# Optimization experiments

Hardware: AMD Instinct MI355X
Metric: run time of the kernel (lower is better)

The kernel has to match this reference:

```python
import jax, jax.numpy as jnp
import numpy as np

D, N, H, DK, DFF, L = 1024, 2048, 8, 128, 4096, 4
LAM = 1.0 / float(np.sqrt(DK))  # attention scale (layer.lam)


def setup_inputs() -> dict:
    key = jax.random.key(0)
    ks = jax.random.split(key, 6)
    s = 1.0 / float(np.sqrt(D))
    X = jax.random.normal(ks[0], (D, N), jnp.float32)
    Q = jax.random.normal(ks[1], (L, H, DK, D), jnp.float32) * s
    K = jax.random.normal(ks[2], (L, H, DK, D), jnp.float32) * s
    V = jax.random.normal(ks[3], (L, H, D, D), jnp.float32) * s
    W1 = jax.random.normal(ks[4], (L, DFF, D), jnp.float32) * s
    b1 = jnp.zeros((L, DFF, 1), jnp.float32)
    W2 = jax.random.normal(ks[5], (L, D, DFF), jnp.float32) * (1.0 / float(np.sqrt(DFF)))
    b2 = jnp.zeros((L, D, 1), jnp.float32)
    return {"X": X, "Q": Q, "K": K, "V": V, "W1": W1, "b1": b1, "W2": W2, "b2": b2}


def _layer(X, p):
    Q, K, V, W1, b1, W2, b2 = p
    # Batched multi-head attention; original loops heads and sums outputs.
    QX = jnp.einsum('hkd,dn->hkn', Q, X)          # [H, DK, N]
    KX = jnp.einsum('hkd,dn->hkn', K, X)          # [H, DK, N]
    scores = jnp.einsum('hkn,hkm->hnm', QX, KX) * LAM  # [H, N, N]
    A = jax.nn.softmax(scores, axis=1)            # torch softmax(dim=0) over [N, N]
    VX = jnp.einsum('hed,dn->hen', V, X)          # [H, D, N]
    Y = jnp.einsum('hen,hnm->em', VX, A)          # sum over heads -> [D, N]
    X = X + Y
    Hh = jax.nn.relu(W1 @ X + b1)                 # [DFF, N]
    return X + W2 @ Hh + b2


def reference(X, Q, K, V, W1, b1, W2, b2):
    def step(carry, p):
        return _layer(carry, p), None
    Xf, _ = jax.lax.scan(step, X, (Q, K, V, W1, b1, W2, b2))
    return Xf
```

## Files before the change

kernel.cpp:

```cpp
#include <hip/hip_runtime.h>

typedef unsigned short u16;
typedef _Float16 f16;
typedef _Float16 fh8 __attribute__((ext_vector_type(8)));
typedef float f32x4 __attribute__((ext_vector_type(4)));

#define cD   1024
#define cN   2048
#define cH   8
#define cDK  128
#define cDFF 4096
#define cL   4
#define LAM_ 0.08838834764831845f
#define QKSC 64.0f

__device__ __forceinline__ u16 f2h(float f) {
    union { f16 h; u16 u; } x; x.h = (f16)f; return x.u;
}
__device__ __forceinline__ float h2f(u16 u) {
    union { u16 u; f16 h; } x; x.u = u; return (float)x.h;
}
__device__ __forceinline__ void split_fh(float v, u16& h, u16& l) {
    h = f2h(v);
    l = f2h(v - h2f(h));
}

__device__ __forceinline__ void async_cp16(const u16* gsrc, u16* ldst) {
    __builtin_amdgcn_global_load_lds(
        (const __attribute__((address_space(1))) unsigned int*)gsrc,
        (__attribute__((address_space(3))) unsigned int*)(unsigned int)(unsigned long long)ldst,
        16, 0, 0);
}

__global__ void cast_split4(const float* __restrict__ s, u16* __restrict__ h,
                            u16* __restrict__ l, int n4, float sc) {
    int i = blockIdx.x * 256 + threadIdx.x;
    if (i < n4) {
        float4 v = ((const float4*)s)[i];
        v.x *= sc; v.y *= sc; v.z *= sc; v.w *= sc;
        ushort4 hh, ll;
        split_fh(v.x, hh.x, ll.x);
        split_fh(v.y, hh.y, ll.y);
        split_fh(v.z, hh.z, ll.z);
        split_fh(v.w, hh.w, ll.w);
        ((ushort4*)h)[i] = hh;
        if (l) ((ushort4*)l)[i] = ll;
    }
}

__global__ __launch_bounds__(256)
void transpose_f32(const float* __restrict__ in, float* __restrict__ out, int R, int C) {
    __shared__ float t[32][33];
    const int bx = blockIdx.x * 32;
    const int by = blockIdx.y * 32;
    const int tx = threadIdx.x & 31, ty = threadIdx.x >> 5;
#pragma unroll
    for (int yy = 0; yy < 32; yy += 8)
        t[ty + yy][tx] = in[(long)(by + ty + yy) * C + bx + tx];
    __syncthreads();
#pragma unroll
    for (int yy = 0; yy < 32; yy += 8)
        out[(long)(bx + ty + yy) * R + by + tx] = t[tx][ty + yy];
}

__global__ __launch_bounds__(256)
void softmax_rows(const float* __restrict__ S, u16* __restrict__ Ph) {
    const long base = (long)blockIdx.x * cN;
    const float4* s4 = (const float4*)(S + base);
    const int tid = threadIdx.x;
    float4 v0 = s4[tid];
    float4 v1 = s4[tid + 256];
    float mx = fmaxf(fmaxf(fmaxf(v0.x, v0.y), fmaxf(v0.z, v0.w)),
                     fmaxf(fmaxf(v1.x, v1.y), fmaxf(v1.z, v1.w)));
    __shared__ float rm[256], rl[256];
    rm[tid] = mx; __syncthreads();
    for (int w = 128; w > 0; w >>= 1) {
        if (tid < w) rm[tid] = fmaxf(rm[tid], rm[tid + w]);
        __syncthreads();
    }
    mx = rm[0];
    float l = __expf(v0.x - mx) + __expf(v0.y - mx) + __expf(v0.z - mx) + __expf(v0.w - mx)
            + __expf(v1.x - mx) + __expf(v1.y - mx) + __expf(v1.z - mx) + __expf(v1.w - mx);
    rl[tid] = l; __syncthreads();
    for (int w = 128; w > 0; w >>= 1) {
        if (tid < w) rl[tid] += rl[tid + w];
        __syncthreads();
    }
    const float inv = 1.0f / rl[0];
    ushort4 a, b;
    a.x = f2h(__expf(v0.x - mx) * inv);
    a.y = f2h(__expf(v0.y - mx) * inv);
    a.z = f2h(__expf(v0.z - mx) * inv);
    a.w = f2h(__expf(v0.w - mx) * inv);
    b.x = f2h(__expf(v1.x - mx) * inv);
    b.y = f2h(__expf(v1.y - mx) * inv);
    b.z = f2h(__expf(v1.z - mx) * inv);
    b.w = f2h(__expf(v1.w - mx) * inv);
    ((ushort4*)(Ph + base))[tid] = a;
    ((ushort4*)(Ph + base))[tid + 256] = b;
}

template<int ALO, int BLO, int DBUF>
__global__ __launch_bounds__(256)
void gemm_split(const u16* __restrict__ Ah, const u16* __restrict__ Al, int lda, long bsA,
                const u16* __restrict__ Bh, const u16* __restrict__ Bl, int ldb, long bsB,
                float* __restrict__ Cf, u16* __restrict__ Cbh, u16* __restrict__ Cbl,
                int ldc, long bsC,
                int M, int N, int K, int SK,
                float alpha, int mode, int relu, const float* __restrict__ biasN)
{
    const int g = blockIdx.z / SK;
    const int s = blockIdx.z % SK;
    const long za = (long)g * bsA + (long)s * K;
    const long zb = (long)g * bsB + (long)s * K;
    Ah += za; Bh += zb;
    if constexpr (ALO) Al += za;
    if constexpr (BLO) Bl += zb;
    if (s != 0) biasN = nullptr;

    __shared__ __align__(16) u16 Ash[128 * 32];
    __shared__ __align__(16) u16 Bsh[128 * 32];
    __shared__ __align__(16) u16 Asl[ALO ? 128 * 32 : 8];
    __shared__ __align__(16) u16 Bsl[BLO ? 128 * 32 : 8];
    __shared__ __align__(16) u16 Ash1[DBUF ? 128 * 32 : 8];
    __shared__ __align__(16) u16 Bsh1[DBUF ? 128 * 32 : 8];

    const int tid  = threadIdx.x;
    const int lane = tid & 63;
    const int wave = tid >> 6;
    const int wm = (wave >> 1) * 64;
    const int wn = (wave & 1) * 64;

    const int nbx = gridDim.x;
    const int nwg = nbx * (int)gridDim.y;
    int wg = blockIdx.y * nbx + blockIdx.x;
    {
        const int qq = nwg >> 3, rr = nwg & 7;
        const int xcd = wg & 7, lid = wg >> 3;
        wg = (xcd < rr ? xcd * (qq + 1) : rr * (qq + 1) + (xcd - rr) * qq) + lid;
    }
    const int m0 = (wg / nbx) * 128;
    const int n0 = (wg % nbx) * 128;

    const int srow = lane >> 2;
    const int scol = (((lane & 3) ^ (srow & 3)) * 8);
    const int q = lane >> 4;
    const int r = lane & 15;
    const int fcol = ((q ^ (r & 3)) * 8);

    f32x4 acc[4][4];
#pragma unroll
    for (int i = 0; i < 4; ++i)
#pragma unroll
        for (int j = 0; j < 4; ++j)
            acc[i][j] = f32x4{0.f, 0.f, 0.f, 0.f};

    if constexpr (DBUF) {
        auto stage = [&](u16* SA, u16* SB, int k0) {
#pragma unroll
            for (int p = 0; p < 2; ++p) {
                const int c = p * 4 + wave;
                const int grow = c * 16 + srow;
                async_cp16(Ah + (long)(m0 + grow) * lda + k0 + scol, SA + c * 512);
                async_cp16(Bh + (long)(n0 + grow) * ldb + k0 + scol, SB + c * 512);
            }
        };
        auto compute = [&](const u16* SA, const u16* SB) {
            fh8 af[4], bf[4];
#pragma unroll
            for (int i = 0; i < 4; ++i) af[i] = *(const fh8*)(SA + (wm + i * 16 + r) * 32 + fcol);
#pragma unroll
            for (int j = 0; j < 4; ++j) bf[j] = *(const fh8*)(SB + (wn + j * 16 + r) * 32 + fcol);
#pragma unroll
            for (int i = 0; i < 4; ++i)
#pragma unroll
                for (int j = 0; j < 4; ++j)
                    acc[i][j] = __builtin_amdgcn_mfma_f32_16x16x32_f16(af[i], bf[j], acc[i][j], 0, 0, 0);
        };

        stage(Ash, Bsh, 0);
        for (int k0 = 0; k0 < K; k0 += 64) {
            stage(Ash1, Bsh1, k0 + 32);
            asm volatile("s_waitcnt vmcnt(4)" ::: "memory");
            __builtin_amdgcn_s_barrier();
            asm volatile("" ::: "memory");
            compute(Ash, Bsh);
            asm volatile("" ::: "memory");
            __builtin_amdgcn_s_barrier();
            if (k0 + 64 < K) {
                stage(Ash, Bsh, k0 + 64);
                asm volatile("s_waitcnt vmcnt(4)" ::: "memory");
            } else {
                asm volatile("s_waitcnt vmcnt(0)" ::: "memory");
            }
            __builtin_amdgcn_s_barrier();
            asm volatile("" ::: "memory");
            compute(Ash1, Bsh1);
            asm volatile("" ::: "memory");
            __builtin_amdgcn_s_barrier();
        }
    } else {
        for (int k0 = 0; k0 < K; k0 += 32) {
#pragma unroll
            for (int p = 0; p < 2; ++p) {
                const int c = p * 4 + wave;
                const int grow = c * 16 + srow;
                const long aoff = (long)(m0 + grow) * lda + k0 + scol;
                const long boff = (long)(n0 + grow) * ldb + k0 + scol;
                async_cp16(Ah + aoff, Ash + c * 512);
                if constexpr (ALO) async_cp16(Al + aoff, Asl + c * 512);
                async_cp16(Bh + boff, Bsh + c * 512);
                if constexpr (BLO) async_cp16(Bl + boff, Bsl + c * 512);
            }
            __syncthreads();

            fh8 afh[4], afl[4], bfh[4], bfl[4];
#pragma unroll
            for (int i = 0; i < 4; ++i) {
                const int ra = (wm + i * 16 + r) * 32 + fcol;
                afh[i] = *(const fh8*)(Ash + ra);
                if constexpr (ALO) afl[i] = *(const fh8*)(Asl + ra);
            }
#pragma unroll
            for (int j = 0; j < 4; ++j) {
                const int rb = (wn + j * 16 + r) * 32 + fcol;
                bfh[j] = *(const fh8*)(Bsh + rb);
                if constexpr (BLO) bfl[j] = *(const fh8*)(Bsl + rb);
            }
#pragma unroll
            for (int i = 0; i < 4; ++i)
#pragma unroll
                for (int j = 0; j < 4; ++j) {
                    acc[i][j] = __builtin_amdgcn_mfma_f32_16x16x32_f16(afh[i], bfh[j], acc[i][j], 0, 0, 0);
                    if constexpr (BLO)
                        acc[i][j] = __builtin_amdgcn_mfma_f32_16x16x32_f16(afh[i], bfl[j], acc[i][j], 0, 0, 0);
                    if constexpr (ALO)
                        acc[i][j] = __builtin_amdgcn_mfma_f32_16x16x32_f16(afl[i], bfh[j], acc[i][j], 0, 0, 0);
                }
            __syncthreads();
        }
    }

#pragma unroll
    for (int i = 0; i < 4; ++i) {
#pragma unroll
        for (int j = 0; j < 4; ++j) {
            const int col = n0 + wn + j * 16 + r;
#pragma unroll
            for (int t = 0; t < 4; ++t) {
                const int row = m0 + wm + i * 16 + q * 4 + t;
                float v = acc[i][j][t] * alpha;
                if (biasN) v += biasN[col];
                if (relu)  v = fmaxf(v, 0.f);
                const long idx = (long)g * bsC + (long)row * ldc + col;
                if (mode == 0) {
                    if (Cbl) { u16 a, b; split_fh(v, a, b); Cbh[idx] = a; Cbl[idx] = b; }
                    else     { Cbh[idx] = f2h(v); }
                } else if (mode == 1) {
                    Cf[idx] = v;
                } else {
                    unsafeAtomicAdd(&Cf[idx], v);
                }
            }
        }
    }
}

static inline void launch_gemm(hipStream_t st, int split3,
                               const u16* Ah, const u16* Al, int lda, long bsA,
                               const u16* Bh, const u16* Bl, int ldb, long bsB,
                               float* Cf, u16* Cbh, u16* Cbl, int ldc, long bsC,
                               int M, int N, int K, int Gz, int SK,
                               float alpha, int mode, int relu, const float* biasN)
{
    dim3 grid(N / 128, M / 128, Gz * SK), block(256);
    if (split3)
        gemm_split<1, 1, 0><<<grid, block, 0, st>>>(Ah, Al, lda, bsA, Bh, Bl, ldb, bsB,
                                                    Cf, Cbh, Cbl, ldc, bsC,
                                                    M, N, K, SK, alpha, mode, relu, biasN);
    else
        gemm_split<0, 0, 1><<<grid, block, 0, st>>>(Ah, Al, lda, bsA, Bh, Bl, ldb, bsB,
                                                    Cf, Cbh, Cbl, ldc, bsC,
                                                    M, N, K, SK, alpha, mode, relu, biasN);
}

static inline void launch_cast(hipStream_t st, const float* s, u16* h, u16* l, long n,
                               float sc = 1.0f) {
    int n4 = (int)(n / 4);
    cast_split4<<<dim3((n4 + 255) / 256), dim3(256), 0, st>>>(s, h, l, n4, sc);
}

extern "C" void kernel_launch(void* const* d_in, const int* in_sizes, int n_in,
                              void* d_out, int out_size, void* d_ws, size_t ws_size,
                              hipStream_t stream)
{
    const float* Xin = (const float*)d_in[0];
    const float* Qw  = (const float*)d_in[1];
    const float* Kw  = (const float*)d_in[2];
    const float* Vw  = (const float*)d_in[3];
    const float* W1w = (const float*)d_in[4];
    const float* b1w = (const float*)d_in[5];
    const float* W2w = (const float*)d_in[6];
    const float* b2w = (const float*)d_in[7];
    float* Xout = (float*)d_out;

    int G = 1;
    if      (ws_size >= 402653184ull + 1048576) G = 8;
    else if (ws_size >= 218103808ull + 1048576) G = 4;
    else if (ws_size >= 125829120ull + 1048576) G = 2;

    char* base = (char*)d_ws;
    size_t off = 0;
    auto carve = [&](size_t bytes) {
        char* p = base + off; off = (off + bytes + 255) & ~(size_t)255; return p;
    };
    float* Xt     = (float*)carve((size_t)cN * cD * 4);
    u16*   XbT_h  = (u16*)carve((size_t)cN * cD * 2);
    u16*   XbT_l  = (u16*)carve((size_t)cN * cD * 2);
    u16*   QKXT_h = (u16*)carve((size_t)2 * cN * cD * 2);
    u16*   QKXT_l = (u16*)carve((size_t)2 * cN * cD * 2);
    u16*   W1_h   = QKXT_h;
    const size_t r2 = off;
    float* ST   = (float*)carve((size_t)G * cN * cN * 4);
    u16*   P_h  = (u16*)carve((size_t)G * cN * cN * 2);
    u16*   P_l  = (u16*)carve((size_t)G * cN * cN * 2);
    u16*   Vb_h = (u16*)carve((size_t)G * cD * cD * 2);
    u16*   Vb_l = (u16*)carve((size_t)G * cD * cD * 2);
    u16*   VX_h = (u16*)carve((size_t)G * cD * cN * 2);
    u16*   VX_l = (u16*)carve((size_t)G * cD * cN * 2);
    (void)P_l; (void)Vb_l; (void)VX_l;
    off = r2;
    u16*   QKb_h = (u16*)carve((size_t)2 * cH * cDK * cD * 2);
    u16*   QKb_l = (u16*)carve((size_t)2 * cH * cDK * cD * 2);
    off = r2;
    u16*   H1_h = (u16*)carve((size_t)cN * cDFF * 2);
    u16*   H1_l = (u16*)carve((size_t)cN * cDFF * 2);
    u16*   W2_h = (u16*)carve((size_t)cD * cDFF * 2);
    (void)H1_l;

    const u16* QXT_h = QKXT_h;
    const u16* QXT_l = QKXT_l;
    const u16* KXT_h = QKXT_h + (size_t)cN * cD;
    const u16* KXT_l = QKXT_l + (size_t)cN * cD;

    transpose_f32<<<dim3(cN / 32, cD / 32), dim3(256), 0, stream>>>(Xin, Xt, cD, cN);

    const int SKy = (G >= 4) ? 1 : (G == 2 ? 2 : 4);
    const float stalpha = LAM_ / (QKSC * QKSC);

    for (int l = 0; l < cL; ++l) {
        launch_cast(stream, Xt, XbT_h, XbT_l, (long)cN * cD);

        const long nQK = (long)cH * cDK * cD;
        launch_cast(stream, Qw + (long)l * nQK, QKb_h, QKb_l, nQK, QKSC);
        launch_cast(stream, Kw + (long)l * nQK, QKb_h + nQK, QKb_l + nQK, nQK, QKSC);

        launch_gemm(stream, 1, XbT_h, XbT_l, cD, 0,
                    QKb_h, QKb_l, cD, nQK,
                    nullptr, QKXT_h, QKXT_l, cD, (long)cN * cD,
                    cN, cD, cD, 2, 1, 1.f, 0, 0, nullptr);

        for (int g0 = 0; g0 < cH; g0 += G) {
            launch_gemm(stream, 1, KXT_h + (long)g0 * cDK, KXT_l + (long)g0 * cDK, cD, cDK,
                        QXT_h + (long)g0 * cDK, QXT_l + (long)g0 * cDK, cD, cDK,
                        ST, nullptr, nullptr, cN, (long)cN * cN,
                        cN, cN, cDK, G, 1, stalpha, 1, 0, nullptr);
            softmax_rows<<<dim3(G * cN), dim3(256), 0, stream>>>(ST, P_h);

            const long nV = (long)cD * cD;
            launch_cast(stream, Vw + ((long)l * cH + g0) * nV, Vb_h, nullptr, (long)G * nV);
            launch_gemm(stream, 0, Vb_h, nullptr, cD, nV,
                        XbT_h, nullptr, cD, 0,
                        nullptr, VX_h, nullptr, cN, (long)cD * cN,
                        cD, cN, cD, G, 1, 1.f, 0, 0, nullptr);
            launch_gemm(stream, 0, P_h, nullptr, cN, (long)cN * cN,
                        VX_h, nullptr, cN, (long)cD * cN,
                        Xt, nullptr, nullptr, cD, 0,
                        cN, cD, cN / SKy, G, SKy, 1.f, 3, 0, nullptr);
        }

        launch_cast(stream, Xt, XbT_h, nullptr, (long)cN * cD);
        const long nW = (long)cDFF * cD;
        launch_cast(stream, W1w + (long)l * nW, W1_h, nullptr, nW);
        launch_gemm(stream, 0, XbT_h, nullptr, cD, 0,
                    W1_h, nullptr, cD, 0,
                    nullptr, H1_h, nullptr, cDFF, 0,
                    cN, cDFF, cD, 1, 1, 1.f, 0, 1, b1w + (long)l * cDFF);
        launch_cast(stream, W2w + (long)l * nW, W2_h, nullptr, nW);
        launch_gemm(stream, 0, H1_h, nullptr, cDFF, 0,
                    W2_h, nullptr, cDFF, 0,
                    Xt, nullptr, nullptr, cD, 0,
                    cN, cD, cDFF / 4, 1, 4, 1.f, 3, 0, b2w + (long)l * cD);
    }

    transpose_f32<<<dim3(cD / 32, cN / 32), dim3(256), 0, stream>>>(Xt, Xout, cN, cD);

    (void)in_sizes; (void)n_in; (void)out_size;
}
```

Before: 2.079 ms.

## Triple-buffer the fp16 GEMM shared-memory pipeline with two-stage prefetch

Replaces the double-buffered K loop in the single-precision-split GEMM with a three-buffer ring that keeps two tiles in flight ahead of the one being computed. Wait counts are adjusted so each step waits only for the oldest outstanding load. The aim is to hide more global-memory latency behind MFMA work. In exchange it uses more LDS per block, which may reduce occupancy.

```diff
diff --git a/kernel.cpp b/kernel.cpp
--- a/kernel.cpp
+++ b/kernel.cpp
@@ -124,6 +124,8 @@
     __shared__ __align__(16) u16 Bsl[BLO ? 128 * 32 : 8];
     __shared__ __align__(16) u16 Ash1[DBUF ? 128 * 32 : 8];
     __shared__ __align__(16) u16 Bsh1[DBUF ? 128 * 32 : 8];
+    __shared__ __align__(16) u16 Ash2[DBUF ? 128 * 32 : 8];
+    __shared__ __align__(16) u16 Bsh2[DBUF ? 128 * 32 : 8];
 
     const int tid  = threadIdx.x;
     const int lane = tid & 63;
@@ -156,6 +158,7 @@
             acc[i][j] = f32x4{0.f, 0.f, 0.f, 0.f};
 
     if constexpr (DBUF) {
+        const int nt = K >> 5;
         auto stage = [&](u16* SA, u16* SB, int k0) {
 #pragma unroll
             for (int p = 0; p < 2; ++p) {
@@ -177,27 +180,33 @@
                 for (int j = 0; j < 4; ++j)
                     acc[i][j] = __builtin_amdgcn_mfma_f32_16x16x32_f16(af[i], bf[j], acc[i][j], 0, 0, 0);
         };
-
-        stage(Ash, Bsh, 0);
-        for (int k0 = 0; k0 < K; k0 += 64) {
-            stage(Ash1, Bsh1, k0 + 32);
-            asm volatile("s_waitcnt vmcnt(4)" ::: "memory");
-            __builtin_amdgcn_s_barrier();
-            asm volatile("" ::: "memory");
-            compute(Ash, Bsh);
-            asm volatile("" ::: "memory");
-            __builtin_amdgcn_s_barrier();
-            if (k0 + 64 < K) {
-                stage(Ash, Bsh, k0 + 64);
+        auto step = [&](const u16* CA, const u16* CB, u16* PA, u16* PB, int pk) {
+            if (pk < nt) {
+                stage(PA, PB, pk * 32);
+                asm volatile("s_waitcnt vmcnt(8)" ::: "memory");
+            } else if (pk - 1 < nt) {
                 asm volatile("s_waitcnt vmcnt(4)" ::: "memory");
             } else {
                 asm volatile("s_waitcnt vmcnt(0)" ::: "memory");
             }
             __builtin_amdgcn_s_barrier();
-            asm volatile("" ::: "memory");
-            compute(Ash1, Bsh1);
-            asm volatile("" ::: "memory");
+            compute(CA, CB);
             __builtin_amdgcn_s_barrier();
+        };
+
+        stage(Ash,  Bsh,  0);
+        stage(Ash1, Bsh1, 32);
+        int t = 0;
+        for (; t + 3 <= nt; t += 3) {
+            step(Ash,  Bsh,  Ash2, Bsh2, t + 2);
+            step(Ash1, Bsh1, Ash,  Bsh,  t + 3);
+            step(Ash2, Bsh2, Ash1, Bsh1, t + 4);
+        }
+        if (nt - t == 2) {
+            step(Ash,  Bsh,  Ash2, Bsh2, t + 2);
+            step(Ash1, Bsh1, Ash2, Bsh2, t + 3);
+        } else if (nt - t == 1) {
+            step(Ash,  Bsh,  Ash2, Bsh2, t + 2);
         }
     } else {
         for (int k0 = 0; k0 < K; k0 += 32) {
```

New measurement: 2.031 ms. 2.3% less time.
